# Optimization experiments

Measured on AMD Instinct MI355X. Metric: run time of the kernel, lower is better.

The kernel has to match this reference:

```python
import jax, jax.numpy as jnp
import numpy as np

N_NODES = 100000


def setup_inputs() -> dict:
    key = jax.random.key(0)
    k_x, k_src, k_dst, k_w = jax.random.split(key, 4)
    X = jax.random.normal(k_x, (N_NODES, 128), dtype=jnp.float32)
    src = jax.random.randint(k_src, (3200000,), 0, N_NODES, dtype=jnp.int64)
    dst = jax.random.randint(k_dst, (3200000,), 0, N_NODES, dtype=jnp.int64)
    # Linear(2*in_channels=256 -> out_channels=128); kaiming-ish scale
    W = jax.random.normal(k_w, (256, 128), dtype=jnp.float32) * (1.0 / np.sqrt(256.0))
    b = jnp.zeros((128,), dtype=jnp.float32)
    return {"X": X, "src": src, "dst": dst, "W": W, "b": b}


def reference(X, src, dst, W, b):
    # G.v2v(X, aggr='mean'): scatter-mean of neighbor features over edges
    msg = X[src]                                              # [E, d] gather
    summed = jax.ops.segment_sum(msg, dst, num_segments=N_NODES)  # [N, d]
    deg = jax.ops.segment_sum(jnp.ones_like(dst, dtype=X.dtype), dst,
                              num_segments=N_NODES)           # [N]
    X_nbr = summed / jnp.maximum(deg, 1.0)[:, None]           # mean, safe for deg=0
    # concat self + neighbor mean, linear, relu (dropout is eval-mode no-op)
    H = jnp.concatenate([X, X_nbr], axis=1)                   # [N, 2d]
    out = jax.nn.relu(H @ W + b)                              # [N, out]
    return out
```

## Files before the change

kernel.cpp:

```cpp
#include <hip/hip_runtime.h>
#include <cstddef>
#include <cstdint>


#define NODES_PER_BLOCK 16
#define PART_SHIFT 8
#define PART_SZ 256
#define MAXP 448
#define CHUNK 4096
#define CAPP 8704
#define CAPN 96

typedef __attribute__((ext_vector_type(8))) short bf16x8;
typedef __attribute__((ext_vector_type(4))) float f32x4;

__device__ __forceinline__ int clampi(int v, int hi) {
    v = v < 0 ? 0 : v;
    return v >= hi ? hi - 1 : v;
}

__device__ __forceinline__ unsigned short bf16_rne(float f) {
    unsigned int u = __float_as_uint(f);
    unsigned int r = (u + 0x7FFFu + ((u >> 16) & 1u)) >> 16;
    return (unsigned short)r;
}

__device__ __forceinline__ unsigned pack2(float a, float b) {
    return (unsigned)bf16_rne(a) | ((unsigned)bf16_rne(b) << 16);
}

__device__ __forceinline__ void acc_bf16x8(float* a, uint4 r) {
    a[0] += __uint_as_float(r.x << 16);
    a[1] += __uint_as_float(r.x & 0xFFFF0000u);
    a[2] += __uint_as_float(r.y << 16);
    a[3] += __uint_as_float(r.y & 0xFFFF0000u);
    a[4] += __uint_as_float(r.z << 16);
    a[5] += __uint_as_float(r.z & 0xFFFF0000u);
    a[6] += __uint_as_float(r.w << 16);
    a[7] += __uint_as_float(r.w & 0xFFFF0000u);
}

__device__ __forceinline__ int wave_excl_scan64(int v, int lane) {
    int x = v;
#pragma unroll
    for (int off = 1; off < 64; off <<= 1) {
        int y = __shfl_up(x, off, 64);
        if (lane >= off) x += y;
    }
    return x - v;
}

__global__ void zero_cursors(int* __restrict__ c, int P) {
    int i = blockIdx.x * blockDim.x + threadIdx.x;
    if (i < P) c[i] = 0;
}

__device__ void do_xw_block(int xb,
    const float* __restrict__ X, unsigned short* __restrict__ Xb, int total4,
    const float* __restrict__ W, unsigned short* __restrict__ Wswz)
{
    int i = xb * 256 + threadIdx.x;
    if (i < 256 * 128) {
        int k = i >> 7, n = i & 127;
        int kk = k >> 5, q = (k >> 3) & 3, j = k & 7;
        int cg = n >> 4, nn = n & 15;
        int lane = q * 16 + nn;
        Wswz[((size_t)(kk * 8 + cg) * 64 + lane) * 8 + j] =
            bf16_rne(W[(size_t)k * 128 + n]);
    }
    if (i < total4) {
        float4 v = *(const float4*)(X + (size_t)i * 4);
        ushort4 o;
        o.x = bf16_rne(v.x); o.y = bf16_rne(v.y);
        o.z = bf16_rne(v.z); o.w = bf16_rne(v.w);
        *(ushort4*)(Xb + (size_t)i * 4) = o;
    }
}

__global__ __launch_bounds__(256) void pre1(
    const int* __restrict__ src, const int* __restrict__ dst,
    int* __restrict__ cursors, unsigned long long* __restrict__ parts,
    int E, int N, int P, int nPart1, int capp,
    const float* __restrict__ X, unsigned short* __restrict__ Xb, int total4,
    const float* __restrict__ W, unsigned short* __restrict__ Wswz)
{
    if ((int)blockIdx.x >= nPart1) {
        do_xw_block((int)blockIdx.x - nPart1, X, Xb, total4, W, Wswz);
        return;
    }
    __shared__ unsigned long long sbuf[CHUNK];
    __shared__ int hist[MAXP], base_s[MAXP], gbase[MAXP];
    const int tid = threadIdx.x;
    const int c0  = blockIdx.x * CHUNK;
    int cnt = E - c0; if (cnt > CHUNK) cnt = CHUNK;

    for (int i = tid; i < P; i += 256) hist[i] = 0;
    __syncthreads();

    int s[16], d[16], r[16];
#pragma unroll
    for (int k = 0; k < 16; ++k) {
        int i = k * 256 + tid;
        if (i < cnt) {
            int e = c0 + i;
            d[k] = clampi(dst[e], N);
            s[k] = clampi(src[e], N);
            r[k] = atomicAdd(&hist[d[k] >> PART_SHIFT], 1);
        } else {
            d[k] = -1; s[k] = 0; r[k] = 0;
        }
    }
    __syncthreads();

    if (tid < 64) {
        int pref[7]; int run = 0;
#pragma unroll
        for (int k2 = 0; k2 < 7; ++k2) {
            int idx = tid * 7 + k2;
            int v = (idx < P) ? hist[idx] : 0;
            pref[k2] = run; run += v;
        }
        int lx = wave_excl_scan64(run, tid);
#pragma unroll
        for (int k2 = 0; k2 < 7; ++k2) {
            int idx = tid * 7 + k2;
            if (idx < P) base_s[idx] = pref[k2] + lx;
        }
    }
    __syncthreads();

    for (int i = tid; i < P; i += 256) {
        int c = hist[i];
        gbase[i] = (c > 0) ? atomicAdd(&cursors[i], c) : 0;
    }
    __syncthreads();

#pragma unroll
    for (int k = 0; k < 16; ++k) {
        if (d[k] >= 0) {
            int p = d[k] >> PART_SHIFT;
            sbuf[base_s[p] + r[k]] =
                ((unsigned long long)(unsigned)d[k] << 32) | (unsigned)s[k];
        }
    }
    __syncthreads();

    for (int i = tid; i < cnt; i += 256) {
        unsigned long long rec = sbuf[i];
        int p = ((int)(rec >> 32)) >> PART_SHIFT;
        int gidx = gbase[p] + (i - base_s[p]);
        if (gidx < capp) parts[(size_t)p * capp + gidx] = rec;
    }
}

__global__ __launch_bounds__(128) void gather_gemm(
    const unsigned short* __restrict__ Xb,
    const unsigned long long* __restrict__ parts,
    const int* __restrict__ cursors,
    int capp,
    const unsigned short* __restrict__ Wswz,
    const float* __restrict__ bias,
    float* __restrict__ out, int N, int nwg)
{
    __shared__ unsigned short Hb[NODES_PER_BLOCK][256];
    __shared__ int lsrc[NODES_PER_BLOCK][CAPN];
    __shared__ int ldeg[NODES_PER_BLOCK];
    __shared__ int nextn;
    const int tid = threadIdx.x;

    const int bid  = (int)blockIdx.x;
    const int q8   = nwg >> 3;
    const int work = (bid & 7) * q8 + (bid >> 3);
    const int p    = work >> 4;
    const int g    = work & 15;
    const int n0   = p * PART_SZ + g * NODES_PER_BLOCK;
    if (n0 >= N) return;

    if (tid < NODES_PER_BLOCK) ldeg[tid] = 0;
    if (tid == 0) nextn = 0;
    __syncthreads();

    {
        int cnt = cursors[p]; if (cnt > capp) cnt = capp;
        const unsigned long long* prec = parts + (size_t)p * capp;
        int i = tid;
        for (; i + 128 < cnt; i += 256) {
            unsigned long long r0 = prec[i];
            unsigned long long r1 = prec[i + 128];
            int dl0 = ((int)(r0 >> 32)) & (PART_SZ - 1);
            int dl1 = ((int)(r1 >> 32)) & (PART_SZ - 1);
            if ((dl0 >> 4) == g) {
                int r = atomicAdd(&ldeg[dl0 & 15], 1);
                if (r < CAPN) lsrc[dl0 & 15][r] = (int)(r0 & 0xFFFFFFFFu);
            }
            if ((dl1 >> 4) == g) {
                int r = atomicAdd(&ldeg[dl1 & 15], 1);
                if (r < CAPN) lsrc[dl1 & 15][r] = (int)(r1 & 0xFFFFFFFFu);
            }
        }
        for (; i < cnt; i += 128) {
            unsigned long long r0 = prec[i];
            int dl0 = ((int)(r0 >> 32)) & (PART_SZ - 1);
            if ((dl0 >> 4) == g) {
                int r = atomicAdd(&ldeg[dl0 & 15], 1);
                if (r < CAPN) lsrc[dl0 & 15][r] = (int)(r0 & 0xFFFFFFFFu);
            }
        }
    }
    __syncthreads();

    {
        const int lane63 = tid & 63;
        const int sub    = tid & 15;
        const int f0     = sub * 8;
        int vtake = 0;
        if (sub == 0) vtake = atomicAdd(&nextn, 1);
        int v = __shfl(vtake, lane63 & 48, 64);
        while (v < NODES_PER_BLOCK) {
            const int n = n0 + v;
            if (n < N) {
                const int dg  = ldeg[v];
                const int dgl = dg < CAPN ? dg : CAPN;
                const int* brow = lsrc[v];
                float acc[8] = {0.f, 0.f, 0.f, 0.f, 0.f, 0.f, 0.f, 0.f};
                int t = 0;
                for (; t + 8 <= dgl; t += 8) {
                    int i0 = brow[t],     i1 = brow[t + 1];
                    int i2 = brow[t + 2], i3 = brow[t + 3];
                    int i4 = brow[t + 4], i5 = brow[t + 5];
                    int i6 = brow[t + 6], i7 = brow[t + 7];
                    uint4 r0 = *(const uint4*)(Xb + (size_t)i0 * 128 + f0);
                    uint4 r1 = *(const uint4*)(Xb + (size_t)i1 * 128 + f0);
                    uint4 r2 = *(const uint4*)(Xb + (size_t)i2 * 128 + f0);
                    uint4 r3 = *(const uint4*)(Xb + (size_t)i3 * 128 + f0);
                    uint4 r4 = *(const uint4*)(Xb + (size_t)i4 * 128 + f0);
                    uint4 r5 = *(const uint4*)(Xb + (size_t)i5 * 128 + f0);
                    uint4 r6 = *(const uint4*)(Xb + (size_t)i6 * 128 + f0);
                    uint4 r7 = *(const uint4*)(Xb + (size_t)i7 * 128 + f0);
                    acc_bf16x8(acc, r0); acc_bf16x8(acc, r1);
                    acc_bf16x8(acc, r2); acc_bf16x8(acc, r3);
                    acc_bf16x8(acc, r4); acc_bf16x8(acc, r5);
                    acc_bf16x8(acc, r6); acc_bf16x8(acc, r7);
                }
                for (; t + 4 <= dgl; t += 4) {
                    int i0 = brow[t],     i1 = brow[t + 1];
                    int i2 = brow[t + 2], i3 = brow[t + 3];
                    uint4 r0 = *(const uint4*)(Xb + (size_t)i0 * 128 + f0);
                    uint4 r1 = *(const uint4*)(Xb + (size_t)i1 * 128 + f0);
                    uint4 r2 = *(const uint4*)(Xb + (size_t)i2 * 128 + f0);
                    uint4 r3 = *(const uint4*)(Xb + (size_t)i3 * 128 + f0);
                    acc_bf16x8(acc, r0); acc_bf16x8(acc, r1);
                    acc_bf16x8(acc, r2); acc_bf16x8(acc, r3);
                }
                for (; t < dgl; ++t) {
                    uint4 r0 = *(const uint4*)(Xb + (size_t)brow[t] * 128 + f0);
                    acc_bf16x8(acc, r0);
                }
                const float inv = 1.0f / fmaxf((float)dg, 1.0f);
                *(uint4*)&Hb[v][f0] = *(const uint4*)(Xb + (size_t)n * 128 + f0);
                uint4 mo;
                mo.x = pack2(acc[0] * inv, acc[1] * inv);
                mo.y = pack2(acc[2] * inv, acc[3] * inv);
                mo.z = pack2(acc[4] * inv, acc[5] * inv);
                mo.w = pack2(acc[6] * inv, acc[7] * inv);
                *(uint4*)&Hb[v][128 + f0] = mo;
            }
            if (sub == 0) vtake = atomicAdd(&nextn, 1);
            v = __shfl(vtake, lane63 & 48, 64);
        }
    }
    __syncthreads();

    const int lane = tid & 63;
    const int wv   = tid >> 6;
    const int m    = lane & 15;
    const int quad = lane >> 4;
    f32x4 acc0 = {0.f, 0.f, 0.f, 0.f};
    f32x4 acc1 = {0.f, 0.f, 0.f, 0.f};
    f32x4 acc2 = {0.f, 0.f, 0.f, 0.f};
    f32x4 acc3 = {0.f, 0.f, 0.f, 0.f};
#pragma unroll
    for (int kk = 0; kk < 8; ++kk) {
        bf16x8 a = *(const bf16x8*)&Hb[m][kk * 32 + quad * 8];
        const unsigned short* wp =
            Wswz + ((size_t)(kk * 8 + wv * 4) * 64 + lane) * 8;
        bf16x8 b0 = *(const bf16x8*)(wp);
        bf16x8 b1 = *(const bf16x8*)(wp + 64 * 8);
        bf16x8 b2 = *(const bf16x8*)(wp + 2 * 64 * 8);
        bf16x8 b3 = *(const bf16x8*)(wp + 3 * 64 * 8);
        acc0 = __builtin_amdgcn_mfma_f32_16x16x32_bf16(a, b0, acc0, 0, 0, 0);
        acc1 = __builtin_amdgcn_mfma_f32_16x16x32_bf16(a, b1, acc1, 0, 0, 0);
        acc2 = __builtin_amdgcn_mfma_f32_16x16x32_bf16(a, b2, acc2, 0, 0, 0);
        acc3 = __builtin_amdgcn_mfma_f32_16x16x32_bf16(a, b3, acc3, 0, 0, 0);
    }
    f32x4 accs[4] = {acc0, acc1, acc2, acc3};
#pragma unroll
    for (int c = 0; c < 4; ++c) {
        int feat = wv * 64 + c * 16 + m;
        float bv = bias[feat];
#pragma unroll
        for (int r = 0; r < 4; ++r) {
            int node = n0 + quad * 4 + r;
            if (node < N)
                out[(size_t)node * 128 + feat] = fmaxf(accs[c][r] + bv, 0.f);
        }
    }
}

static inline size_t align256(size_t x) { return (x + 255) & ~(size_t)255; }

extern "C" void kernel_launch(void* const* d_in, const int* in_sizes, int n_in,
                              void* d_out, int out_size, void* d_ws, size_t ws_size,
                              hipStream_t stream) {
    const float* X    = (const float*)d_in[0];
    const int*   src  = (const int*)d_in[1];
    const int*   dst  = (const int*)d_in[2];
    const float* W    = (const float*)d_in[3];
    const float* bias = (const float*)d_in[4];
    float* out = (float*)d_out;

    const int N = in_sizes[0] / 128;
    const int E = in_sizes[1];
    const int P = (N + PART_SZ - 1) >> PART_SHIFT;

    char* base = (char*)d_ws;
    size_t o_cursors = 0;
    size_t o_wswz    = align256((size_t)P * 4);
    size_t o_xb      = o_wswz + align256((size_t)256 * 128 * 2);
    size_t o_parts   = o_xb   + align256((size_t)N * 128 * 2);

    int capp = CAPP;
    {
        size_t avail = (ws_size > o_parts) ? (ws_size - o_parts) : 0;
        size_t fit = avail / ((size_t)P * 8);
        if (fit < (size_t)capp) capp = (int)fit;
    }

    int* cursors              = (int*)(base + o_cursors);
    unsigned short* Wswz      = (unsigned short*)(base + o_wswz);
    unsigned short* Xb        = (unsigned short*)(base + o_xb);
    unsigned long long* parts = (unsigned long long*)(base + o_parts);

    const int nPart1 = (E + CHUNK - 1) / CHUNK;
    const int total4 = (N * 128) / 4;
    const int nXw    = (total4 + 255) / 256;
    const int nwg    = P * 16;

    zero_cursors<<<(P + 255) / 256, 256, 0, stream>>>(cursors, P);
    pre1<<<nPart1 + nXw, 256, 0, stream>>>(
        src, dst, cursors, parts, E, N, P, nPart1, capp, X, Xb, total4, W, Wswz);
    gather_gemm<<<nwg, 128, 0, stream>>>(
        Xb, parts, cursors, capp, Wswz, bias, out, N, nwg);
}
```

Before: 307.3 us.

## Scatter partition records directly to global, drop LDS staging and dynamic node queue

The partition pre-pass no longer stages records in shared memory with a prefix scan. It builds a histogram, reserves global slots, then re-reads src/dst with int4 loads and writes each record straight to its partition using decrementing shared atomics. Chunk size and block size double to 8192 edges and 512 threads. The gather kernel replaces its atomic work-stealing node queue with a static two-nodes-per-16-lane-group assignment. The trade is fewer syncs and less LDS against rereading the indices, global writes that are no longer contiguous per partition, and possible load imbalance across node degrees.

```diff
diff --git a/kernel.cpp b/kernel.cpp
--- a/kernel.cpp
+++ b/kernel.cpp
@@ -7,7 +7,7 @@
 #define PART_SHIFT 8
 #define PART_SZ 256
 #define MAXP 448
-#define CHUNK 4096
+#define CHUNK 8192
 #define CAPP 8704
 #define CAPN 96
 
@@ -40,16 +40,6 @@
     a[7] += __uint_as_float(r.w & 0xFFFF0000u);
 }
 
-__device__ __forceinline__ int wave_excl_scan64(int v, int lane) {
-    int x = v;
-#pragma unroll
-    for (int off = 1; off < 64; off <<= 1) {
-        int y = __shfl_up(x, off, 64);
-        if (lane >= off) x += y;
-    }
-    return x - v;
-}
-
 __global__ void zero_cursors(int* __restrict__ c, int P) {
     int i = blockIdx.x * blockDim.x + threadIdx.x;
     if (i < P) c[i] = 0;
@@ -59,7 +49,7 @@
     const float* __restrict__ X, unsigned short* __restrict__ Xb, int total4,
     const float* __restrict__ W, unsigned short* __restrict__ Wswz)
 {
-    int i = xb * 256 + threadIdx.x;
+    int i = xb * 512 + threadIdx.x;
     if (i < 256 * 128) {
         int k = i >> 7, n = i & 127;
         int kk = k >> 5, q = (k >> 3) & 3, j = k & 7;
@@ -77,7 +67,7 @@
     }
 }
 
-__global__ __launch_bounds__(256) void pre1(
+__global__ __launch_bounds__(512) void pre1(
     const int* __restrict__ src, const int* __restrict__ dst,
     int* __restrict__ cursors, unsigned long long* __restrict__ parts,
     int E, int N, int P, int nPart1, int capp,
@@ -88,68 +78,68 @@
         do_xw_block((int)blockIdx.x - nPart1, X, Xb, total4, W, Wswz);
         return;
     }
-    __shared__ unsigned long long sbuf[CHUNK];
-    __shared__ int hist[MAXP], base_s[MAXP], gbase[MAXP];
+    __shared__ int hist[MAXP], gbase[MAXP];
     const int tid = threadIdx.x;
     const int c0  = blockIdx.x * CHUNK;
-    int cnt = E - c0; if (cnt > CHUNK) cnt = CHUNK;
-
-    for (int i = tid; i < P; i += 256) hist[i] = 0;
-    __syncthreads();
-
-    int s[16], d[16], r[16];
-#pragma unroll
-    for (int k = 0; k < 16; ++k) {
-        int i = k * 256 + tid;
-        if (i < cnt) {
-            int e = c0 + i;
-            d[k] = clampi(dst[e], N);
-            s[k] = clampi(src[e], N);
-            r[k] = atomicAdd(&hist[d[k] >> PART_SHIFT], 1);
+    const int cnt = (E - c0 < CHUNK) ? (E - c0) : CHUNK;
+
+    for (int i = tid; i < P; i += 512) hist[i] = 0;
+    __syncthreads();
+
+#pragma unroll
+    for (int g = 0; g < 4; ++g) {
+        int i0 = (g * 512 + tid) * 4;
+        if (i0 + 4 <= cnt) {
+            int4 d4 = *(const int4*)(dst + c0 + i0);
+            atomicAdd(&hist[clampi(d4.x, N) >> PART_SHIFT], 1);
+            atomicAdd(&hist[clampi(d4.y, N) >> PART_SHIFT], 1);
+            atomicAdd(&hist[clampi(d4.z, N) >> PART_SHIFT], 1);
+            atomicAdd(&hist[clampi(d4.w, N) >> PART_SHIFT], 1);
         } else {
-            d[k] = -1; s[k] = 0; r[k] = 0;
-        }
-    }
-    __syncthreads();
-
-    if (tid < 64) {
-        int pref[7]; int run = 0;
-#pragma unroll
-        for (int k2 = 0; k2 < 7; ++k2) {
-            int idx = tid * 7 + k2;
-            int v = (idx < P) ? hist[idx] : 0;
-            pref[k2] = run; run += v;
-        }
-        int lx = wave_excl_scan64(run, tid);
-#pragma unroll
-        for (int k2 = 0; k2 < 7; ++k2) {
-            int idx = tid * 7 + k2;
-            if (idx < P) base_s[idx] = pref[k2] + lx;
-        }
-    }
-    __syncthreads();
-
-    for (int i = tid; i < P; i += 256) {
+            for (int i = i0; i < cnt; ++i)
+                atomicAdd(&hist[clampi(dst[c0 + i], N) >> PART_SHIFT], 1);
+        }
+    }
+    __syncthreads();
+
+    for (int i = tid; i < P; i += 512) {
         int c = hist[i];
         gbase[i] = (c > 0) ? atomicAdd(&cursors[i], c) : 0;
     }
     __syncthreads();
 
 #pragma unroll
-    for (int k = 0; k < 16; ++k) {
-        if (d[k] >= 0) {
-            int p = d[k] >> PART_SHIFT;
-            sbuf[base_s[p] + r[k]] =
-                ((unsigned long long)(unsigned)d[k] << 32) | (unsigned)s[k];
-        }
-    }
-    __syncthreads();
-
-    for (int i = tid; i < cnt; i += 256) {
-        unsigned long long rec = sbuf[i];
-        int p = ((int)(rec >> 32)) >> PART_SHIFT;
-        int gidx = gbase[p] + (i - base_s[p]);
-        if (gidx < capp) parts[(size_t)p * capp + gidx] = rec;
+    for (int g = 0; g < 4; ++g) {
+        int i0 = (g * 512 + tid) * 4;
+        if (i0 + 4 <= cnt) {
+            int4 d4 = *(const int4*)(dst + c0 + i0);
+            int4 s4 = *(const int4*)(src + c0 + i0);
+            int dd[4] = {clampi(d4.x, N), clampi(d4.y, N),
+                         clampi(d4.z, N), clampi(d4.w, N)};
+            int ss[4] = {clampi(s4.x, N), clampi(s4.y, N),
+                         clampi(s4.z, N), clampi(s4.w, N)};
+#pragma unroll
+            for (int k = 0; k < 4; ++k) {
+                int p = dd[k] >> PART_SHIFT;
+                int r = atomicAdd(&hist[p], -1) - 1;
+                int slot = gbase[p] + r;
+                if (slot < capp)
+                    parts[(size_t)p * capp + slot] =
+                        ((unsigned long long)(unsigned)dd[k] << 32) |
+                        (unsigned)ss[k];
+            }
+        } else {
+            for (int i = i0; i < cnt; ++i) {
+                int d = clampi(dst[c0 + i], N);
+                int s = clampi(src[c0 + i], N);
+                int p = d >> PART_SHIFT;
+                int r = atomicAdd(&hist[p], -1) - 1;
+                int slot = gbase[p] + r;
+                if (slot < capp)
+                    parts[(size_t)p * capp + slot] =
+                        ((unsigned long long)(unsigned)d << 32) | (unsigned)s;
+            }
+        }
     }
 }
 
@@ -165,7 +155,6 @@
     __shared__ unsigned short Hb[NODES_PER_BLOCK][256];
     __shared__ int lsrc[NODES_PER_BLOCK][CAPN];
     __shared__ int ldeg[NODES_PER_BLOCK];
-    __shared__ int nextn;
     const int tid = threadIdx.x;
 
     const int bid  = (int)blockIdx.x;
@@ -177,7 +166,6 @@
     if (n0 >= N) return;
 
     if (tid < NODES_PER_BLOCK) ldeg[tid] = 0;
-    if (tid == 0) nextn = 0;
     __syncthreads();
 
     {
@@ -210,63 +198,58 @@
     __syncthreads();
 
     {
-        const int lane63 = tid & 63;
-        const int sub    = tid & 15;
-        const int f0     = sub * 8;
-        int vtake = 0;
-        if (sub == 0) vtake = atomicAdd(&nextn, 1);
-        int v = __shfl(vtake, lane63 & 48, 64);
-        while (v < NODES_PER_BLOCK) {
+        const int sub = tid & 15;
+        const int grp = tid >> 4;
+        const int f0  = sub * 8;
+        for (int ii = 0; ii < 2; ++ii) {
+            const int v = grp * 2 + ii;
             const int n = n0 + v;
-            if (n < N) {
-                const int dg  = ldeg[v];
-                const int dgl = dg < CAPN ? dg : CAPN;
-                const int* brow = lsrc[v];
-                float acc[8] = {0.f, 0.f, 0.f, 0.f, 0.f, 0.f, 0.f, 0.f};
-                int t = 0;
-                for (; t + 8 <= dgl; t += 8) {
-                    int i0 = brow[t],     i1 = brow[t + 1];
-                    int i2 = brow[t + 2], i3 = brow[t + 3];
-                    int i4 = brow[t + 4], i5 = brow[t + 5];
-                    int i6 = brow[t + 6], i7 = brow[t + 7];
-                    uint4 r0 = *(const uint4*)(Xb + (size_t)i0 * 128 + f0);
-                    uint4 r1 = *(const uint4*)(Xb + (size_t)i1 * 128 + f0);
-                    uint4 r2 = *(const uint4*)(Xb + (size_t)i2 * 128 + f0);
-                    uint4 r3 = *(const uint4*)(Xb + (size_t)i3 * 128 + f0);
-                    uint4 r4 = *(const uint4*)(Xb + (size_t)i4 * 128 + f0);
-                    uint4 r5 = *(const uint4*)(Xb + (size_t)i5 * 128 + f0);
-                    uint4 r6 = *(const uint4*)(Xb + (size_t)i6 * 128 + f0);
-                    uint4 r7 = *(const uint4*)(Xb + (size_t)i7 * 128 + f0);
-                    acc_bf16x8(acc, r0); acc_bf16x8(acc, r1);
-                    acc_bf16x8(acc, r2); acc_bf16x8(acc, r3);
-                    acc_bf16x8(acc, r4); acc_bf16x8(acc, r5);
-                    acc_bf16x8(acc, r6); acc_bf16x8(acc, r7);
-                }
-                for (; t + 4 <= dgl; t += 4) {
-                    int i0 = brow[t],     i1 = brow[t + 1];
-                    int i2 = brow[t + 2], i3 = brow[t + 3];
-                    uint4 r0 = *(const uint4*)(Xb + (size_t)i0 * 128 + f0);
-                    uint4 r1 = *(const uint4*)(Xb + (size_t)i1 * 128 + f0);
-                    uint4 r2 = *(const uint4*)(Xb + (size_t)i2 * 128 + f0);
-                    uint4 r3 = *(const uint4*)(Xb + (size_t)i3 * 128 + f0);
-                    acc_bf16x8(acc, r0); acc_bf16x8(acc, r1);
-                    acc_bf16x8(acc, r2); acc_bf16x8(acc, r3);
-                }
-                for (; t < dgl; ++t) {
-                    uint4 r0 = *(const uint4*)(Xb + (size_t)brow[t] * 128 + f0);
-                    acc_bf16x8(acc, r0);
-                }
-                const float inv = 1.0f / fmaxf((float)dg, 1.0f);
-                *(uint4*)&Hb[v][f0] = *(const uint4*)(Xb + (size_t)n * 128 + f0);
-                uint4 mo;
-                mo.x = pack2(acc[0] * inv, acc[1] * inv);
-                mo.y = pack2(acc[2] * inv, acc[3] * inv);
-                mo.z = pack2(acc[4] * inv, acc[5] * inv);
-                mo.w = pack2(acc[6] * inv, acc[7] * inv);
-                *(uint4*)&Hb[v][128 + f0] = mo;
-            }
-            if (sub == 0) vtake = atomicAdd(&nextn, 1);
-            v = __shfl(vtake, lane63 & 48, 64);
+            if (n >= N) continue;
+            const int dg  = ldeg[v];
+            const int dgl = dg < CAPN ? dg : CAPN;
+            const int* brow = lsrc[v];
+            float acc[8] = {0.f, 0.f, 0.f, 0.f, 0.f, 0.f, 0.f, 0.f};
+            int t = 0;
+            for (; t + 8 <= dgl; t += 8) {
+                int i0 = brow[t],     i1 = brow[t + 1];
+                int i2 = brow[t + 2], i3 = brow[t + 3];
+                int i4 = brow[t + 4], i5 = brow[t + 5];
+                int i6 = brow[t + 6], i7 = brow[t + 7];
+                uint4 r0 = *(const uint4*)(Xb + (size_t)i0 * 128 + f0);
+                uint4 r1 = *(const uint4*)(Xb + (size_t)i1 * 128 + f0);
+                uint4 r2 = *(const uint4*)(Xb + (size_t)i2 * 128 + f0);
+                uint4 r3 = *(const uint4*)(Xb + (size_t)i3 * 128 + f0);
+                uint4 r4 = *(const uint4*)(Xb + (size_t)i4 * 128 + f0);
+                uint4 r5 = *(const uint4*)(Xb + (size_t)i5 * 128 + f0);
+                uint4 r6 = *(const uint4*)(Xb + (size_t)i6 * 128 + f0);
+                uint4 r7 = *(const uint4*)(Xb + (size_t)i7 * 128 + f0);
+                acc_bf16x8(acc, r0); acc_bf16x8(acc, r1);
+                acc_bf16x8(acc, r2); acc_bf16x8(acc, r3);
+                acc_bf16x8(acc, r4); acc_bf16x8(acc, r5);
+                acc_bf16x8(acc, r6); acc_bf16x8(acc, r7);
+            }
+            for (; t + 4 <= dgl; t += 4) {
+                int i0 = brow[t],     i1 = brow[t + 1];
+                int i2 = brow[t + 2], i3 = brow[t + 3];
+                uint4 r0 = *(const uint4*)(Xb + (size_t)i0 * 128 + f0);
+                uint4 r1 = *(const uint4*)(Xb + (size_t)i1 * 128 + f0);
+                uint4 r2 = *(const uint4*)(Xb + (size_t)i2 * 128 + f0);
+                uint4 r3 = *(const uint4*)(Xb + (size_t)i3 * 128 + f0);
+                acc_bf16x8(acc, r0); acc_bf16x8(acc, r1);
+                acc_bf16x8(acc, r2); acc_bf16x8(acc, r3);
+            }
+            for (; t < dgl; ++t) {
+                uint4 r0 = *(const uint4*)(Xb + (size_t)brow[t] * 128 + f0);
+                acc_bf16x8(acc, r0);
+            }
+            const float inv = 1.0f / fmaxf((float)dg, 1.0f);
+            *(uint4*)&Hb[v][f0] = *(const uint4*)(Xb + (size_t)n * 128 + f0);
+            uint4 mo;
+            mo.x = pack2(acc[0] * inv, acc[1] * inv);
+            mo.y = pack2(acc[2] * inv, acc[3] * inv);
+            mo.z = pack2(acc[4] * inv, acc[5] * inv);
+            mo.w = pack2(acc[6] * inv, acc[7] * inv);
+            *(uint4*)&Hb[v][128 + f0] = mo;
         }
     }
     __syncthreads();
@@ -343,11 +326,11 @@
 
     const int nPart1 = (E + CHUNK - 1) / CHUNK;
     const int total4 = (N * 128) / 4;
-    const int nXw    = (total4 + 255) / 256;
+    const int nXw    = (total4 + 511) / 512;
     const int nwg    = P * 16;
 
     zero_cursors<<<(P + 255) / 256, 256, 0, stream>>>(cursors, P);
-    pre1<<<nPart1 + nXw, 256, 0, stream>>>(
+    pre1<<<nPart1 + nXw, 512, 0, stream>>>(
         src, dst, cursors, parts, E, N, P, nPart1, capp, X, Xb, total4, W, Wswz);
     gather_gemm<<<nwg, 128, 0, stream>>>(
         Xb, parts, cursors, capp, Wswz, bias, out, N, nwg);
```

Measured after the change: 327.7 us. 1.07x slower.

## Replace atomic cursor partitioning with histogram-scan-scatter and 32-node gather blocks

Applied to the files above, without the earlier changes.

Partitioning edges by destination now takes three passes: a per-chunk histogram kernel fused with the bf16 conversion, a per-partition scan kernel that computes chunk offsets, and a scatter kernel that writes records at those offsets. This replaces the global atomic cursors and the zeroing kernel, and makes edge order within each partition deterministic. The gather/GEMM kernel now handles 32 nodes per 256-thread block with a static node assignment in place of the dynamic atomic work queue, which halves the number of times each partition's records are rescanned. The cost is an extra pass over dst and two more launches, and static node assignment may balance uneven degrees less well.

```diff
diff --git a/kernel.cpp b/kernel.cpp
--- a/kernel.cpp
+++ b/kernel.cpp
@@ -3,7 +3,7 @@
 #include <cstdint>
 
 
-#define NODES_PER_BLOCK 16
+#define NODES_PER_BLOCK 32
 #define PART_SHIFT 8
 #define PART_SZ 256
 #define MAXP 448
@@ -48,11 +48,6 @@
         if (lane >= off) x += y;
     }
     return x - v;
-}
-
-__global__ void zero_cursors(int* __restrict__ c, int P) {
-    int i = blockIdx.x * blockDim.x + threadIdx.x;
-    if (i < P) c[i] = 0;
 }
 
 __device__ void do_xw_block(int xb,
@@ -77,39 +72,106 @@
     }
 }
 
-__global__ __launch_bounds__(256) void pre1(
-    const int* __restrict__ src, const int* __restrict__ dst,
-    int* __restrict__ cursors, unsigned long long* __restrict__ parts,
-    int E, int N, int P, int nPart1, int capp,
+__global__ __launch_bounds__(256) void hist_convert(
+    const int* __restrict__ dst, int* __restrict__ counts,
+    int E, int N, int P, int nChunk,
     const float* __restrict__ X, unsigned short* __restrict__ Xb, int total4,
     const float* __restrict__ W, unsigned short* __restrict__ Wswz)
 {
-    if ((int)blockIdx.x >= nPart1) {
-        do_xw_block((int)blockIdx.x - nPart1, X, Xb, total4, W, Wswz);
+    const int bid = (int)blockIdx.x;
+    if (bid >= nChunk) {
+        do_xw_block(bid - nChunk, X, Xb, total4, W, Wswz);
         return;
     }
+    __shared__ int hist[MAXP];
+    const int tid = threadIdx.x;
+    const int c0  = bid * CHUNK;
+    const int cnt = (E - c0 < CHUNK) ? (E - c0) : CHUNK;
+
+    for (int i = tid; i < P; i += 256) hist[i] = 0;
+    __syncthreads();
+
+#pragma unroll
+    for (int g = 0; g < 4; ++g) {
+        int i0 = (g * 256 + tid) * 4;
+        if (i0 + 4 <= cnt) {
+            int4 d4 = *(const int4*)(dst + c0 + i0);
+            atomicAdd(&hist[clampi(d4.x, N) >> PART_SHIFT], 1);
+            atomicAdd(&hist[clampi(d4.y, N) >> PART_SHIFT], 1);
+            atomicAdd(&hist[clampi(d4.z, N) >> PART_SHIFT], 1);
+            atomicAdd(&hist[clampi(d4.w, N) >> PART_SHIFT], 1);
+        } else {
+            for (int i = i0; i < cnt && i < i0 + 4; ++i)
+                atomicAdd(&hist[clampi(dst[c0 + i], N) >> PART_SHIFT], 1);
+        }
+    }
+    __syncthreads();
+    for (int i = tid; i < P; i += 256)
+        counts[(size_t)i * nChunk + bid] = hist[i];
+}
+
+__global__ __launch_bounds__(64) void scan_bases(
+    int* __restrict__ counts, int* __restrict__ pcnt, int nChunk)
+{
+    const int p    = (int)blockIdx.x;
+    const int lane = (int)threadIdx.x;
+    int* row = counts + (size_t)p * nChunk;
+    int carry = 0;
+    for (int j = 0; j < nChunk; j += 64) {
+        int idx = j + lane;
+        int v = (idx < nChunk) ? row[idx] : 0;
+        int ex = wave_excl_scan64(v, lane);
+        if (idx < nChunk) row[idx] = carry + ex;
+        carry += __shfl(ex + v, 63, 64);
+    }
+    if (lane == 0) pcnt[p] = carry;
+}
+
+__global__ __launch_bounds__(256) void scatter_parts(
+    const int* __restrict__ src, const int* __restrict__ dst,
+    const int* __restrict__ counts, unsigned long long* __restrict__ parts,
+    int E, int N, int P, int nChunk, int capp)
+{
     __shared__ unsigned long long sbuf[CHUNK];
     __shared__ int hist[MAXP], base_s[MAXP], gbase[MAXP];
+    const int bid = (int)blockIdx.x;
     const int tid = threadIdx.x;
-    const int c0  = blockIdx.x * CHUNK;
-    int cnt = E - c0; if (cnt > CHUNK) cnt = CHUNK;
-
-    for (int i = tid; i < P; i += 256) hist[i] = 0;
+    const int c0  = bid * CHUNK;
+    const int cnt = (E - c0 < CHUNK) ? (E - c0) : CHUNK;
+
+    for (int i = tid; i < P; i += 256) {
+        hist[i] = 0;
+        gbase[i] = counts[(size_t)i * nChunk + bid];
+    }
     __syncthreads();
 
     int s[16], d[16], r[16];
 #pragma unroll
-    for (int k = 0; k < 16; ++k) {
-        int i = k * 256 + tid;
-        if (i < cnt) {
-            int e = c0 + i;
-            d[k] = clampi(dst[e], N);
-            s[k] = clampi(src[e], N);
-            r[k] = atomicAdd(&hist[d[k] >> PART_SHIFT], 1);
+    for (int g = 0; g < 4; ++g) {
+        int i0 = (g * 256 + tid) * 4;
+        if (i0 + 4 <= cnt) {
+            int4 d4 = *(const int4*)(dst + c0 + i0);
+            int4 s4 = *(const int4*)(src + c0 + i0);
+            d[g * 4 + 0] = clampi(d4.x, N); s[g * 4 + 0] = clampi(s4.x, N);
+            d[g * 4 + 1] = clampi(d4.y, N); s[g * 4 + 1] = clampi(s4.y, N);
+            d[g * 4 + 2] = clampi(d4.z, N); s[g * 4 + 2] = clampi(s4.z, N);
+            d[g * 4 + 3] = clampi(d4.w, N); s[g * 4 + 3] = clampi(s4.w, N);
         } else {
-            d[k] = -1; s[k] = 0; r[k] = 0;
-        }
-    }
+#pragma unroll
+            for (int k = 0; k < 4; ++k) {
+                int i = i0 + k;
+                if (i < cnt) {
+                    d[g * 4 + k] = clampi(dst[c0 + i], N);
+                    s[g * 4 + k] = clampi(src[c0 + i], N);
+                } else {
+                    d[g * 4 + k] = -1; s[g * 4 + k] = 0;
+                }
+            }
+        }
+    }
+#pragma unroll
+    for (int k = 0; k < 16; ++k)
+        r[k] = (d[k] >= 0) ? atomicAdd(&hist[d[k] >> PART_SHIFT], 1) : 0;
     __syncthreads();
 
     if (tid < 64) {
@@ -126,12 +188,6 @@
             int idx = tid * 7 + k2;
             if (idx < P) base_s[idx] = pref[k2] + lx;
         }
-    }
-    __syncthreads();
-
-    for (int i = tid; i < P; i += 256) {
-        int c = hist[i];
-        gbase[i] = (c > 0) ? atomicAdd(&cursors[i], c) : 0;
     }
     __syncthreads();
 
@@ -148,15 +204,15 @@
     for (int i = tid; i < cnt; i += 256) {
         unsigned long long rec = sbuf[i];
         int p = ((int)(rec >> 32)) >> PART_SHIFT;
-        int gidx = gbase[p] + (i - base_s[p]);
-        if (gidx < capp) parts[(size_t)p * capp + gidx] = rec;
-    }
-}
-
-__global__ __launch_bounds__(128) void gather_gemm(
+        int slot = gbase[p] + (i - base_s[p]);
+        if (slot < capp) parts[(size_t)p * capp + slot] = rec;
+    }
+}
+
+__global__ __launch_bounds__(256) void gather_gemm(
     const unsigned short* __restrict__ Xb,
     const unsigned long long* __restrict__ parts,
-    const int* __restrict__ cursors,
+    const int* __restrict__ pcnt,
     int capp,
     const unsigned short* __restrict__ Wswz,
     const float* __restrict__ bias,
@@ -165,114 +221,109 @@
     __shared__ unsigned short Hb[NODES_PER_BLOCK][256];
     __shared__ int lsrc[NODES_PER_BLOCK][CAPN];
     __shared__ int ldeg[NODES_PER_BLOCK];
-    __shared__ int nextn;
     const int tid = threadIdx.x;
 
     const int bid  = (int)blockIdx.x;
     const int q8   = nwg >> 3;
     const int work = (bid & 7) * q8 + (bid >> 3);
-    const int p    = work >> 4;
-    const int g    = work & 15;
+    const int p    = work >> 3;
+    const int g    = work & 7;
     const int n0   = p * PART_SZ + g * NODES_PER_BLOCK;
     if (n0 >= N) return;
 
     if (tid < NODES_PER_BLOCK) ldeg[tid] = 0;
-    if (tid == 0) nextn = 0;
     __syncthreads();
 
     {
-        int cnt = cursors[p]; if (cnt > capp) cnt = capp;
+        int cnt = pcnt[p]; if (cnt > capp) cnt = capp;
         const unsigned long long* prec = parts + (size_t)p * capp;
         int i = tid;
-        for (; i + 128 < cnt; i += 256) {
+        for (; i + 256 < cnt; i += 512) {
             unsigned long long r0 = prec[i];
-            unsigned long long r1 = prec[i + 128];
+            unsigned long long r1 = prec[i + 256];
             int dl0 = ((int)(r0 >> 32)) & (PART_SZ - 1);
             int dl1 = ((int)(r1 >> 32)) & (PART_SZ - 1);
-            if ((dl0 >> 4) == g) {
-                int r = atomicAdd(&ldeg[dl0 & 15], 1);
-                if (r < CAPN) lsrc[dl0 & 15][r] = (int)(r0 & 0xFFFFFFFFu);
-            }
-            if ((dl1 >> 4) == g) {
-                int r = atomicAdd(&ldeg[dl1 & 15], 1);
-                if (r < CAPN) lsrc[dl1 & 15][r] = (int)(r1 & 0xFFFFFFFFu);
-            }
-        }
-        for (; i < cnt; i += 128) {
+            if ((dl0 >> 5) == g) {
+                int r = atomicAdd(&ldeg[dl0 & 31], 1);
+                if (r < CAPN) lsrc[dl0 & 31][r] = (int)(r0 & 0xFFFFFFFFu);
+            }
+            if ((dl1 >> 5) == g) {
+                int r = atomicAdd(&ldeg[dl1 & 31], 1);
+                if (r < CAPN) lsrc[dl1 & 31][r] = (int)(r1 & 0xFFFFFFFFu);
+            }
+        }
+        for (; i < cnt; i += 256) {
             unsigned long long r0 = prec[i];
             int dl0 = ((int)(r0 >> 32)) & (PART_SZ - 1);
-            if ((dl0 >> 4) == g) {
-                int r = atomicAdd(&ldeg[dl0 & 15], 1);
-                if (r < CAPN) lsrc[dl0 & 15][r] = (int)(r0 & 0xFFFFFFFFu);
+            if ((dl0 >> 5) == g) {
+                int r = atomicAdd(&ldeg[dl0 & 31], 1);
+                if (r < CAPN) lsrc[dl0 & 31][r] = (int)(r0 & 0xFFFFFFFFu);
             }
         }
     }
     __syncthreads();
 
     {
-        const int lane63 = tid & 63;
-        const int sub    = tid & 15;
-        const int f0     = sub * 8;
-        int vtake = 0;
-        if (sub == 0) vtake = atomicAdd(&nextn, 1);
-        int v = __shfl(vtake, lane63 & 48, 64);
-        while (v < NODES_PER_BLOCK) {
+        const int sub = tid & 15;
+        const int grp = tid >> 4;
+        const int f0  = sub * 8;
+        for (int ii = 0; ii < 2; ++ii) {
+            const int v = grp * 2 + ii;
             const int n = n0 + v;
-            if (n < N) {
-                const int dg  = ldeg[v];
-                const int dgl = dg < CAPN ? dg : CAPN;
-                const int* brow = lsrc[v];
-                float acc[8] = {0.f, 0.f, 0.f, 0.f, 0.f, 0.f, 0.f, 0.f};
-                int t = 0;
-                for (; t + 8 <= dgl; t += 8) {
-                    int i0 = brow[t],     i1 = brow[t + 1];
-                    int i2 = brow[t + 2], i3 = brow[t + 3];
-                    int i4 = brow[t + 4], i5 = brow[t + 5];
-                    int i6 = brow[t + 6], i7 = brow[t + 7];
-                    uint4 r0 = *(const uint4*)(Xb + (size_t)i0 * 128 + f0);
-                    uint4 r1 = *(const uint4*)(Xb + (size_t)i1 * 128 + f0);
-                    uint4 r2 = *(const uint4*)(Xb + (size_t)i2 * 128 + f0);
-                    uint4 r3 = *(const uint4*)(Xb + (size_t)i3 * 128 + f0);
-                    uint4 r4 = *(const uint4*)(Xb + (size_t)i4 * 128 + f0);
-                    uint4 r5 = *(const uint4*)(Xb + (size_t)i5 * 128 + f0);
-                    uint4 r6 = *(const uint4*)(Xb + (size_t)i6 * 128 + f0);
-                    uint4 r7 = *(const uint4*)(Xb + (size_t)i7 * 128 + f0);
-                    acc_bf16x8(acc, r0); acc_bf16x8(acc, r1);
-                    acc_bf16x8(acc, r2); acc_bf16x8(acc, r3);
-                    acc_bf16x8(acc, r4); acc_bf16x8(acc, r5);
-                    acc_bf16x8(acc, r6); acc_bf16x8(acc, r7);
-                }
-                for (; t + 4 <= dgl; t += 4) {
-                    int i0 = brow[t],     i1 = brow[t + 1];
-                    int i2 = brow[t + 2], i3 = brow[t + 3];
-                    uint4 r0 = *(const uint4*)(Xb + (size_t)i0 * 128 + f0);
-                    uint4 r1 = *(const uint4*)(Xb + (size_t)i1 * 128 + f0);
-                    uint4 r2 = *(const uint4*)(Xb + (size_t)i2 * 128 + f0);
-                    uint4 r3 = *(const uint4*)(Xb + (size_t)i3 * 128 + f0);
-                    acc_bf16x8(acc, r0); acc_bf16x8(acc, r1);
-                    acc_bf16x8(acc, r2); acc_bf16x8(acc, r3);
-                }
-                for (; t < dgl; ++t) {
-                    uint4 r0 = *(const uint4*)(Xb + (size_t)brow[t] * 128 + f0);
-                    acc_bf16x8(acc, r0);
-                }
-                const float inv = 1.0f / fmaxf((float)dg, 1.0f);
-                *(uint4*)&Hb[v][f0] = *(const uint4*)(Xb + (size_t)n * 128 + f0);
-                uint4 mo;
-                mo.x = pack2(acc[0] * inv, acc[1] * inv);
-                mo.y = pack2(acc[2] * inv, acc[3] * inv);
-                mo.z = pack2(acc[4] * inv, acc[5] * inv);
-                mo.w = pack2(acc[6] * inv, acc[7] * inv);
-                *(uint4*)&Hb[v][128 + f0] = mo;
-            }
-            if (sub == 0) vtake = atomicAdd(&nextn, 1);
-            v = __shfl(vtake, lane63 & 48, 64);
+            if (n >= N) continue;
+            const int dg  = ldeg[v];
+            const int dgl = dg < CAPN ? dg : CAPN;
+            const int* brow = lsrc[v];
+            float acc[8] = {0.f, 0.f, 0.f, 0.f, 0.f, 0.f, 0.f, 0.f};
+            int t = 0;
+            for (; t + 8 <= dgl; t += 8) {
+                int i0 = brow[t],     i1 = brow[t + 1];
+                int i2 = brow[t + 2], i3 = brow[t + 3];
+                int i4 = brow[t + 4], i5 = brow[t + 5];
+                int i6 = brow[t + 6], i7 = brow[t + 7];
+                uint4 r0 = *(const uint4*)(Xb + (size_t)i0 * 128 + f0);
+                uint4 r1 = *(const uint4*)(Xb + (size_t)i1 * 128 + f0);
+                uint4 r2 = *(const uint4*)(Xb + (size_t)i2 * 128 + f0);
+                uint4 r3 = *(const uint4*)(Xb + (size_t)i3 * 128 + f0);
+                uint4 r4 = *(const uint4*)(Xb + (size_t)i4 * 128 + f0);
+                uint4 r5 = *(const uint4*)(Xb + (size_t)i5 * 128 + f0);
+                uint4 r6 = *(const uint4*)(Xb + (size_t)i6 * 128 + f0);
+                uint4 r7 = *(const uint4*)(Xb + (size_t)i7 * 128 + f0);
+                acc_bf16x8(acc, r0); acc_bf16x8(acc, r1);
+                acc_bf16x8(acc, r2); acc_bf16x8(acc, r3);
+                acc_bf16x8(acc, r4); acc_bf16x8(acc, r5);
+                acc_bf16x8(acc, r6); acc_bf16x8(acc, r7);
+            }
+            for (; t + 4 <= dgl; t += 4) {
+                int i0 = brow[t],     i1 = brow[t + 1];
+                int i2 = brow[t + 2], i3 = brow[t + 3];
+                uint4 r0 = *(const uint4*)(Xb + (size_t)i0 * 128 + f0);
+                uint4 r1 = *(const uint4*)(Xb + (size_t)i1 * 128 + f0);
+                uint4 r2 = *(const uint4*)(Xb + (size_t)i2 * 128 + f0);
+                uint4 r3 = *(const uint4*)(Xb + (size_t)i3 * 128 + f0);
+                acc_bf16x8(acc, r0); acc_bf16x8(acc, r1);
+                acc_bf16x8(acc, r2); acc_bf16x8(acc, r3);
+            }
+            for (; t < dgl; ++t) {
+                uint4 r0 = *(const uint4*)(Xb + (size_t)brow[t] * 128 + f0);
+                acc_bf16x8(acc, r0);
+            }
+            const float inv = 1.0f / fmaxf((float)dg, 1.0f);
+            *(uint4*)&Hb[v][f0] = *(const uint4*)(Xb + (size_t)n * 128 + f0);
+            uint4 mo;
+            mo.x = pack2(acc[0] * inv, acc[1] * inv);
+            mo.y = pack2(acc[2] * inv, acc[3] * inv);
+            mo.z = pack2(acc[4] * inv, acc[5] * inv);
+            mo.w = pack2(acc[6] * inv, acc[7] * inv);
+            *(uint4*)&Hb[v][128 + f0] = mo;
         }
     }
     __syncthreads();
 
     const int lane = tid & 63;
-    const int wv   = tid >> 6;
+    const int wave = tid >> 6;
+    const int tile = wave >> 1;
+    const int wv2  = wave & 1;
     const int m    = lane & 15;
     const int quad = lane >> 4;
     f32x4 acc0 = {0.f, 0.f, 0.f, 0.f};
@@ -281,9 +332,9 @@
     f32x4 acc3 = {0.f, 0.f, 0.f, 0.f};
 #pragma unroll
     for (int kk = 0; kk < 8; ++kk) {
-        bf16x8 a = *(const bf16x8*)&Hb[m][kk * 32 + quad * 8];
+        bf16x8 a = *(const bf16x8*)&Hb[tile * 16 + m][kk * 32 + quad * 8];
         const unsigned short* wp =
-            Wswz + ((size_t)(kk * 8 + wv * 4) * 64 + lane) * 8;
+            Wswz + ((size_t)(kk * 8 + wv2 * 4) * 64 + lane) * 8;
         bf16x8 b0 = *(const bf16x8*)(wp);
         bf16x8 b1 = *(const bf16x8*)(wp + 64 * 8);
         bf16x8 b2 = *(const bf16x8*)(wp + 2 * 64 * 8);
@@ -296,11 +347,11 @@
     f32x4 accs[4] = {acc0, acc1, acc2, acc3};
 #pragma unroll
     for (int c = 0; c < 4; ++c) {
-        int feat = wv * 64 + c * 16 + m;
+        int feat = wv2 * 64 + c * 16 + m;
         float bv = bias[feat];
 #pragma unroll
         for (int r = 0; r < 4; ++r) {
-            int node = n0 + quad * 4 + r;
+            int node = n0 + tile * 16 + quad * 4 + r;
             if (node < N)
                 out[(size_t)node * 128 + feat] = fmaxf(accs[c][r] + bv, 0.f);
         }
@@ -322,12 +373,14 @@
     const int N = in_sizes[0] / 128;
     const int E = in_sizes[1];
     const int P = (N + PART_SZ - 1) >> PART_SHIFT;
+    const int nChunk = (E + CHUNK - 1) / CHUNK;
 
     char* base = (char*)d_ws;
-    size_t o_cursors = 0;
-    size_t o_wswz    = align256((size_t)P * 4);
-    size_t o_xb      = o_wswz + align256((size_t)256 * 128 * 2);
-    size_t o_parts   = o_xb   + align256((size_t)N * 128 * 2);
+    size_t o_pcnt   = 0;
+    size_t o_counts = align256((size_t)P * 4);
+    size_t o_wswz   = o_counts + align256((size_t)P * nChunk * 4);
+    size_t o_xb     = o_wswz   + align256((size_t)256 * 128 * 2);
+    size_t o_parts  = o_xb     + align256((size_t)N * 128 * 2);
 
     int capp = CAPP;
     {
@@ -336,19 +389,21 @@
         if (fit < (size_t)capp) capp = (int)fit;
     }
 
-    int* cursors              = (int*)(base + o_cursors);
+    int* pcnt                 = (int*)(base + o_pcnt);
+    int* counts               = (int*)(base + o_counts);
     unsigned short* Wswz      = (unsigned short*)(base + o_wswz);
     unsigned short* Xb        = (unsigned short*)(base + o_xb);
     unsigned long long* parts = (unsigned long long*)(base + o_parts);
 
-    const int nPart1 = (E + CHUNK - 1) / CHUNK;
     const int total4 = (N * 128) / 4;
     const int nXw    = (total4 + 255) / 256;
-    const int nwg    = P * 16;
-
-    zero_cursors<<<(P + 255) / 256, 256, 0, stream>>>(cursors, P);
-    pre1<<<nPart1 + nXw, 256, 0, stream>>>(
-        src, dst, cursors, parts, E, N, P, nPart1, capp, X, Xb, total4, W, Wswz);
-    gather_gemm<<<nwg, 128, 0, stream>>>(
-        Xb, parts, cursors, capp, Wswz, bias, out, N, nwg);
-}
+    const int nwg    = P * 8;
+
+    hist_convert<<<nChunk + nXw, 256, 0, stream>>>(
+        dst, counts, E, N, P, nChunk, X, Xb, total4, W, Wswz);
+    scan_bases<<<P, 64, 0, stream>>>(counts, pcnt, nChunk);
+    scatter_parts<<<nChunk, 256, 0, stream>>>(
+        src, dst, counts, parts, E, N, P, nChunk, capp);
+    gather_gemm<<<nwg, 256, 0, stream>>>(
+        Xb, parts, pcnt, capp, Wswz, bias, out, N, nwg);
+}
```

Result: faster. 290.4 us (-5.5%).
